# Kernel optimization log

Measured on AMD Instinct MI355X. Metric: run time of the kernel, lower is better.

The kernel has to match this reference:

```python
import jax, jax.numpy as jnp
import numpy as np

B, F, D, A = 4096, 24, 64, 64

# precompute pairwise field indices (constants derived from num_fields)
_row, _col = np.triu_indices(F, k=1)  # each length F*(F-1)/2 = 276


def setup_inputs() -> dict:
    key = jax.random.key(0)
    k = jax.random.split(key, 5)
    s = 1.0 / np.sqrt(D)
    return {
        "x": jax.random.normal(k[0], (B, F, D), dtype=jnp.float32),
        "Wa": jax.random.normal(k[1], (D, A), dtype=jnp.float32) * s,
        "ba": jnp.zeros((A,), dtype=jnp.float32),
        "Wp": jax.random.normal(k[2], (A, 1), dtype=jnp.float32) * s,
        "bp": jnp.zeros((1,), dtype=jnp.float32),
        "Wfc": jax.random.normal(k[3], (D, 1), dtype=jnp.float32) * s,
        "bfc": jnp.zeros((1,), dtype=jnp.float32),
    }


def reference(x, Wa, ba, Wp, bp, Wfc, bfc):
    row = jnp.asarray(_row)
    col = jnp.asarray(_col)
    # pairwise field products: [B, P, D], P = F*(F-1)/2
    inner_product = x[:, row] * x[:, col]
    # small attention MLP: Linear -> ReLU -> Linear -> softmax over pairs
    h = jax.nn.relu(jnp.einsum("bpd,da->bpa", inner_product, Wa) + ba)
    logits = jnp.einsum("bpa,ao->bpo", h, Wp) + bp            # [B, P, 1]
    attn = jax.nn.softmax(logits, axis=1)                      # softmax over pairs
    # weighted sum over pairs -> [B, D]  (dropouts are 0.0 => identity)
    attn_output = jnp.sum(attn * inner_product, axis=1)
    # final linear -> [B, 1]
    return attn_output @ Wfc + bfc
```

## Files before the change

kernel.cpp:

```cpp
#include <hip/hip_runtime.h>
#include <hip/hip_bf16.h>
#include <math.h>

#define NF 24
#define ND 64
#define NA 64
#define NP 276
#define NPAD 288
#define NTILE 18
#define NT 256
#define BPB 4
#define XPITCH 72

typedef _Float16 f16x8 __attribute__((ext_vector_type(8)));
typedef _Float16 f16x4 __attribute__((ext_vector_type(4)));
typedef float    f32x4 __attribute__((ext_vector_type(4)));

template <int CTRL, int RMASK>
__device__ __forceinline__ float dpp_add_step(float v) {
    int moved = __builtin_amdgcn_update_dpp(0, __float_as_int(v), CTRL, RMASK, 0xf, true);
    return v + __int_as_float(moved);
}
template <int CTRL, int RMASK>
__device__ __forceinline__ float dpp_max_step(float v) {
    int moved = __builtin_amdgcn_update_dpp(__float_as_int(v), __float_as_int(v), CTRL, RMASK, 0xf, false);
    return fmaxf(v, __int_as_float(moved));
}
__device__ __forceinline__ float wave_sum(float v) {
    v = dpp_add_step<0x111, 0xf>(v);
    v = dpp_add_step<0x112, 0xf>(v);
    v = dpp_add_step<0x114, 0xf>(v);
    v = dpp_add_step<0x118, 0xf>(v);
    v = dpp_add_step<0x142, 0xa>(v);
    v = dpp_add_step<0x143, 0xc>(v);
    return __int_as_float(__builtin_amdgcn_readlane(__float_as_int(v), 63));
}
__device__ __forceinline__ float wave_max(float v) {
    v = dpp_max_step<0x111, 0xf>(v);
    v = dpp_max_step<0x112, 0xf>(v);
    v = dpp_max_step<0x114, 0xf>(v);
    v = dpp_max_step<0x118, 0xf>(v);
    v = dpp_max_step<0x142, 0xa>(v);
    v = dpp_max_step<0x143, 0xc>(v);
    return __int_as_float(__builtin_amdgcn_readlane(__float_as_int(v), 63));
}

__global__ __launch_bounds__(64) void afm_prep_kernel(
    const float* __restrict__ Wa,
    const float* __restrict__ Wfc,
    unsigned short* __restrict__ ws)
{
    const int l  = (int)threadIdx.x;
    const int lg = l >> 4, li = l & 15;
    _Float16* waF  = (_Float16*)ws;
    _Float16* wfcF = (_Float16*)(ws + 64 * 64);
    int*      rc   = (int*)(ws + 64 * 64 + 64 * 16);
    #pragma unroll
    for (int nt = 0; nt < 4; ++nt)
        #pragma unroll
        for (int kh = 0; kh < 2; ++kh)
            #pragma unroll
            for (int i = 0; i < 8; ++i) {
                int d = kh * 32 + lg * 8 + i;
                waF[l * 64 + (nt * 2 + kh) * 8 + i] = (_Float16)Wa[d * NA + nt * 16 + li];
            }
    #pragma unroll
    for (int kh = 0; kh < 2; ++kh)
        #pragma unroll
        for (int i = 0; i < 8; ++i) {
            int d = kh * 32 + lg * 8 + i;
            float w = Wfc[d];
            _Float16 hi = (_Float16)w;
            _Float16 lo = (_Float16)(w - (float)hi);
            wfcF[l * 16 + kh * 8 + i] = (li == 0) ? hi : ((li == 1) ? lo : (_Float16)0.f);
        }
    for (int p0 = l; p0 < NPAD; p0 += 64) {
        int r = 0, c = 0;
        if (p0 < NP) {
            int rem = p0;
            while (rem >= NF - 1 - r) { rem -= NF - 1 - r; ++r; }
            c = r + 1 + rem;
        }
        rc[p0] = (r << 16) | c;
    }
}

__global__ __launch_bounds__(NT) void afm_mfma_kernel(
    const float* __restrict__ x,
    const float* __restrict__ ba,
    const float* __restrict__ Wp,
    const float* __restrict__ bfc,
    const unsigned short* __restrict__ ws,
    float* __restrict__ out)
{
    const int tid  = (int)threadIdx.x;
    const int lane = tid & 63;
    const int wid  = tid >> 6;
    const int b    = blockIdx.x * BPB + wid;
    const int lg   = lane >> 4;
    const int li   = lane & 15;

    __shared__ _Float16 xs[BPB][NF][XPITCH];
    __shared__ float    lsums[BPB][NPAD][4];
    __shared__ float    vvs[BPB][NPAD];

    const float4* xb4 = (const float4*)(x + (size_t)b * (NF * ND));
    #pragma unroll
    for (int k = 0; k < 6; ++k) {
        int i = lane + k * 64;
        float4 v = xb4[i];
        f16x4 hv = { (_Float16)v.x, (_Float16)v.y, (_Float16)v.z, (_Float16)v.w };
        *(f16x4*)&xs[wid][i >> 4][(i & 15) * 4] = hv;
    }

    const f16x8* waF  = (const f16x8*)ws;
    const f16x8* wfcF = (const f16x8*)(ws + 64 * 64);
    const int*   rcg  = (const int*)(ws + 64 * 64 + 64 * 16);
    f16x8 WaF[4][2];
    #pragma unroll
    for (int nt = 0; nt < 4; ++nt)
        #pragma unroll
        for (int kh = 0; kh < 2; ++kh)
            WaF[nt][kh] = waF[lane * 8 + nt * 2 + kh];
    f16x8 WfcF[2] = { wfcF[lane * 2 + 0], wfcF[lane * 2 + 1] };

    float ba_t[4][4], wp_t[4][4];
    #pragma unroll
    for (int nt = 0; nt < 4; ++nt)
        #pragma unroll
        for (int j = 0; j < 4; ++j) {
            ba_t[nt][j] = ba[nt * 16 + lg * 4 + j];
            wp_t[nt][j] = Wp[nt * 16 + lg * 4 + j];
        }

    int prt[NTILE];
    #pragma unroll
    for (int t = 0; t < NTILE; ++t) prt[t] = rcg[t * 16 + li];

    asm volatile("s_waitcnt lgkmcnt(0)" ::: "memory");

    f32x4 accP[4], accvP;

    {
        int pr = prt[0];
        int rI = pr >> 16, cI = pr & 0xffff;
        f16x8 Ah[2];
        #pragma unroll
        for (int kh = 0; kh < 2; ++kh) {
            int d0 = kh * 32 + lg * 8;
            f16x8 rv = *(const f16x8*)&xs[wid][rI][d0];
            f16x8 cv = *(const f16x8*)&xs[wid][cI][d0];
            Ah[kh] = rv * cv;
        }
        #pragma unroll
        for (int nt = 0; nt < 4; ++nt) {
            accP[nt] = (f32x4){ba_t[nt][0], ba_t[nt][1], ba_t[nt][2], ba_t[nt][3]};
            accP[nt] = __builtin_amdgcn_mfma_f32_16x16x32_f16(WaF[nt][0], Ah[0], accP[nt], 0, 0, 0);
            accP[nt] = __builtin_amdgcn_mfma_f32_16x16x32_f16(WaF[nt][1], Ah[1], accP[nt], 0, 0, 0);
        }
        accvP = (f32x4){0.f, 0.f, 0.f, 0.f};
        accvP = __builtin_amdgcn_mfma_f32_16x16x32_f16(WfcF[0], Ah[0], accvP, 0, 0, 0);
        accvP = __builtin_amdgcn_mfma_f32_16x16x32_f16(WfcF[1], Ah[1], accvP, 0, 0, 0);
    }

    #pragma unroll
    for (int t = 1; t <= NTILE; ++t) {
        f32x4 accC[4], accvC;
        if (t < NTILE) {
            int pr = prt[t];
            int rI = pr >> 16, cI = pr & 0xffff;
            f16x8 Ah[2];
            #pragma unroll
            for (int kh = 0; kh < 2; ++kh) {
                int d0 = kh * 32 + lg * 8;
                f16x8 rv = *(const f16x8*)&xs[wid][rI][d0];
                f16x8 cv = *(const f16x8*)&xs[wid][cI][d0];
                Ah[kh] = rv * cv;
            }
            #pragma unroll
            for (int nt = 0; nt < 4; ++nt) {
                accC[nt] = (f32x4){ba_t[nt][0], ba_t[nt][1], ba_t[nt][2], ba_t[nt][3]};
                accC[nt] = __builtin_amdgcn_mfma_f32_16x16x32_f16(WaF[nt][0], Ah[0], accC[nt], 0, 0, 0);
                accC[nt] = __builtin_amdgcn_mfma_f32_16x16x32_f16(WaF[nt][1], Ah[1], accC[nt], 0, 0, 0);
            }
            accvC = (f32x4){0.f, 0.f, 0.f, 0.f};
            accvC = __builtin_amdgcn_mfma_f32_16x16x32_f16(WfcF[0], Ah[0], accvC, 0, 0, 0);
            accvC = __builtin_amdgcn_mfma_f32_16x16x32_f16(WfcF[1], Ah[1], accvC, 0, 0, 0);
        }

        {
            float s0 = 0.f, s1 = 0.f, s2 = 0.f, s3 = 0.f;
            #pragma unroll
            for (int j = 0; j < 4; ++j) {
                s0 = fmaf(fmaxf(accP[0][j], 0.f), wp_t[0][j], s0);
                s1 = fmaf(fmaxf(accP[1][j], 0.f), wp_t[1][j], s1);
                s2 = fmaf(fmaxf(accP[2][j], 0.f), wp_t[2][j], s2);
                s3 = fmaf(fmaxf(accP[3][j], 0.f), wp_t[3][j], s3);
            }
            float lsum = (s0 + s1) + (s2 + s3);
            int row = (t - 1) * 16 + li;
            lsums[wid][row][lg] = lsum;
            if (lg == 0)
                vvs[wid][row] = accvP[0] + accvP[1];
        }

        if (t < NTILE) {
            #pragma unroll
            for (int nt = 0; nt < 4; ++nt) accP[nt] = accC[nt];
            accvP = accvC;
        }
    }

    asm volatile("s_waitcnt lgkmcnt(0)" ::: "memory");

    float2 myv[5];
    float m = -INFINITY;
    #pragma unroll
    for (int k = 0; k < 5; ++k) {
        int p = lane + k * 64;
        if (p < NP) {
            float4 ls = *(const float4*)&lsums[wid][p][0];
            float lg4 = (ls.x + ls.y) + (ls.z + ls.w);
            myv[k] = make_float2(lg4, vvs[wid][p]);
            m = fmaxf(m, lg4);
        } else {
            myv[k] = make_float2(-INFINITY, 0.f);
        }
    }
    m = wave_max(m);

    float se = 0.f, sev = 0.f;
    #pragma unroll
    for (int k = 0; k < 5; ++k) {
        int p = lane + k * 64;
        if (p < NP) {
            float e = __expf(myv[k].x - m);
            se += e;
            sev = fmaf(e, myv[k].y, sev);
        }
    }
    se  = wave_sum(se);
    sev = wave_sum(sev);
    if (lane == 0)
        out[b] = sev / se + bfc[0];
}

extern "C" void kernel_launch(void* const* d_in, const int* in_sizes, int n_in,
                              void* d_out, int out_size, void* d_ws, size_t ws_size,
                              hipStream_t stream) {
    const float* x   = (const float*)d_in[0];
    const float* Wa  = (const float*)d_in[1];
    const float* ba  = (const float*)d_in[2];
    const float* Wp  = (const float*)d_in[3];
    const float* Wfc = (const float*)d_in[5];
    const float* bfc = (const float*)d_in[6];
    float* out = (float*)d_out;
    unsigned short* ws = (unsigned short*)d_ws;

    const int B = in_sizes[0] / (NF * ND);
    hipLaunchKernelGGL(afm_prep_kernel, dim3(1), dim3(64), 0, stream, Wa, Wfc, ws);
    hipLaunchKernelGGL(afm_mfma_kernel, dim3(B / BPB), dim3(NT), 0, stream,
                       x, ba, Wp, bfc, ws, out);
}
```

Before: 27.72 us.

## Replace Wfc MFMA projection with fdot2 and compute pair indices in-kernel

The per-pair Wfc projection moves off MFMA (which used a hi/lo split weight tile) onto v_dot2 fp16 instructions with two cross-lane shuffles per tile. The pair row/column table, previously built by the prep kernel and loaded from global memory, is now computed in closed form with a sqrt. Dropping the lo half of the weight split lowers the precision of the projection. The change also adds shuffle and sqrt ALU work in exchange for fewer MFMA issues and fewer global loads.

```diff
diff --git a/kernel.cpp b/kernel.cpp
--- a/kernel.cpp
+++ b/kernel.cpp
@@ -14,6 +14,7 @@
 
 typedef _Float16 f16x8 __attribute__((ext_vector_type(8)));
 typedef _Float16 f16x4 __attribute__((ext_vector_type(4)));
+typedef _Float16 f16x2 __attribute__((ext_vector_type(2)));
 typedef float    f32x4 __attribute__((ext_vector_type(4)));
 
 template <int CTRL, int RMASK>
@@ -45,6 +46,14 @@
     return __int_as_float(__builtin_amdgcn_readlane(__float_as_int(v), 63));
 }
 
+__device__ __forceinline__ float fdot2(f16x2 a, f16x2 b, float c) {
+#if __has_builtin(__builtin_amdgcn_fdot2)
+    return __builtin_amdgcn_fdot2(a, b, c, false);
+#else
+    return fmaf((float)a[1], (float)b[1], fmaf((float)a[0], (float)b[0], c));
+#endif
+}
+
 __global__ __launch_bounds__(64) void afm_prep_kernel(
     const float* __restrict__ Wa,
     const float* __restrict__ Wfc,
@@ -52,9 +61,8 @@
 {
     const int l  = (int)threadIdx.x;
     const int lg = l >> 4, li = l & 15;
-    _Float16* waF  = (_Float16*)ws;
-    _Float16* wfcF = (_Float16*)(ws + 64 * 64);
-    int*      rc   = (int*)(ws + 64 * 64 + 64 * 16);
+    _Float16* waF = (_Float16*)ws;
+    _Float16* wfc = (_Float16*)(ws + 64 * 64);
     #pragma unroll
     for (int nt = 0; nt < 4; ++nt)
         #pragma unroll
@@ -64,25 +72,7 @@
                 int d = kh * 32 + lg * 8 + i;
                 waF[l * 64 + (nt * 2 + kh) * 8 + i] = (_Float16)Wa[d * NA + nt * 16 + li];
             }
-    #pragma unroll
-    for (int kh = 0; kh < 2; ++kh)
-        #pragma unroll
-        for (int i = 0; i < 8; ++i) {
-            int d = kh * 32 + lg * 8 + i;
-            float w = Wfc[d];
-            _Float16 hi = (_Float16)w;
-            _Float16 lo = (_Float16)(w - (float)hi);
-            wfcF[l * 16 + kh * 8 + i] = (li == 0) ? hi : ((li == 1) ? lo : (_Float16)0.f);
-        }
-    for (int p0 = l; p0 < NPAD; p0 += 64) {
-        int r = 0, c = 0;
-        if (p0 < NP) {
-            int rem = p0;
-            while (rem >= NF - 1 - r) { rem -= NF - 1 - r; ++r; }
-            c = r + 1 + rem;
-        }
-        rc[p0] = (r << 16) | c;
-    }
+    wfc[l] = (_Float16)Wfc[l];
 }
 
 __global__ __launch_bounds__(NT) void afm_mfma_kernel(
@@ -114,15 +104,14 @@
     }
 
     const f16x8* waF  = (const f16x8*)ws;
-    const f16x8* wfcF = (const f16x8*)(ws + 64 * 64);
-    const int*   rcg  = (const int*)(ws + 64 * 64 + 64 * 16);
+    const f16x8* wfcP = (const f16x8*)(ws + 64 * 64);
     f16x8 WaF[4][2];
     #pragma unroll
     for (int nt = 0; nt < 4; ++nt)
         #pragma unroll
         for (int kh = 0; kh < 2; ++kh)
             WaF[nt][kh] = waF[lane * 8 + nt * 2 + kh];
-    f16x8 WfcF[2] = { wfcF[lane * 2 + 0], wfcF[lane * 2 + 1] };
+    f16x8 WfcR[2] = { wfcP[lg], wfcP[4 + lg] };
 
     float ba_t[4][4], wp_t[4][4];
     #pragma unroll
@@ -135,11 +124,22 @@
 
     int prt[NTILE];
     #pragma unroll
-    for (int t = 0; t < NTILE; ++t) prt[t] = rcg[t * 16 + li];
+    for (int t = 0; t < NTILE; ++t) {
+        int p = t * 16 + li;
+        if (p > NP - 1) p = NP - 1;
+        float disc = (float)(2209 - 8 * p);
+        int r = (int)((47.0f - sqrtf(disc)) * 0.5f);
+        int S = (r * (47 - r)) >> 1;
+        if (p < S) { --r; S = (r * (47 - r)) >> 1; }
+        else { int S1 = ((r + 1) * (46 - r)) >> 1; if (p >= S1) { ++r; S = S1; } }
+        int c = r + 1 + (p - S);
+        prt[t] = (r << 16) | c;
+    }
 
     asm volatile("s_waitcnt lgkmcnt(0)" ::: "memory");
 
-    f32x4 accP[4], accvP;
+    f32x4 accP[4];
+    float vpP;
 
     {
         int pr = prt[0];
@@ -158,14 +158,22 @@
             accP[nt] = __builtin_amdgcn_mfma_f32_16x16x32_f16(WaF[nt][0], Ah[0], accP[nt], 0, 0, 0);
             accP[nt] = __builtin_amdgcn_mfma_f32_16x16x32_f16(WaF[nt][1], Ah[1], accP[nt], 0, 0, 0);
         }
-        accvP = (f32x4){0.f, 0.f, 0.f, 0.f};
-        accvP = __builtin_amdgcn_mfma_f32_16x16x32_f16(WfcF[0], Ah[0], accvP, 0, 0, 0);
-        accvP = __builtin_amdgcn_mfma_f32_16x16x32_f16(WfcF[1], Ah[1], accvP, 0, 0, 0);
+        float vp = 0.f;
+        #pragma unroll
+        for (int kh = 0; kh < 2; ++kh)
+            #pragma unroll
+            for (int i = 0; i < 4; ++i) {
+                f16x2 a = { Ah[kh][2 * i], Ah[kh][2 * i + 1] };
+                f16x2 w = { WfcR[kh][2 * i], WfcR[kh][2 * i + 1] };
+                vp = fdot2(a, w, vp);
+            }
+        vpP = vp;
     }
 
     #pragma unroll
     for (int t = 1; t <= NTILE; ++t) {
-        f32x4 accC[4], accvC;
+        f32x4 accC[4];
+        float vpC = 0.f;
         if (t < NTILE) {
             int pr = prt[t];
             int rI = pr >> 16, cI = pr & 0xffff;
@@ -183,9 +191,16 @@
                 accC[nt] = __builtin_amdgcn_mfma_f32_16x16x32_f16(WaF[nt][0], Ah[0], accC[nt], 0, 0, 0);
                 accC[nt] = __builtin_amdgcn_mfma_f32_16x16x32_f16(WaF[nt][1], Ah[1], accC[nt], 0, 0, 0);
             }
-            accvC = (f32x4){0.f, 0.f, 0.f, 0.f};
-            accvC = __builtin_amdgcn_mfma_f32_16x16x32_f16(WfcF[0], Ah[0], accvC, 0, 0, 0);
-            accvC = __builtin_amdgcn_mfma_f32_16x16x32_f16(WfcF[1], Ah[1], accvC, 0, 0, 0);
+            float vp = 0.f;
+            #pragma unroll
+            for (int kh = 0; kh < 2; ++kh)
+                #pragma unroll
+                for (int i = 0; i < 4; ++i) {
+                    f16x2 a = { Ah[kh][2 * i], Ah[kh][2 * i + 1] };
+                    f16x2 w = { WfcR[kh][2 * i], WfcR[kh][2 * i + 1] };
+                    vp = fdot2(a, w, vp);
+                }
+            vpC = vp;
         }
 
         {
@@ -200,14 +215,17 @@
             float lsum = (s0 + s1) + (s2 + s3);
             int row = (t - 1) * 16 + li;
             lsums[wid][row][lg] = lsum;
+            float vv = vpP;
+            vv += __shfl_xor(vv, 16);
+            vv += __shfl_xor(vv, 32);
             if (lg == 0)
-                vvs[wid][row] = accvP[0] + accvP[1];
+                vvs[wid][row] = vv;
         }
 
         if (t < NTILE) {
             #pragma unroll
             for (int nt = 0; nt < 4; ++nt) accP[nt] = accC[nt];
-            accvP = accvC;
+            vpP = vpC;
         }
     }
 
```

Result: slower. 33.52 us (+21.0%).
